# Optimization experiments

Measured on AMD Instinct MI355X. Metric: run time of the kernel, lower is better.

The kernel has to match this reference:

```python
import jax, jax.numpy as jnp
import numpy as np

B, N, F, T = 16, 1024, 32, 12
K, FC, FT, TS, D = 3, 64, 64, 1, 16
THETA_THR = 0.6
LN_EPS = 1e-5


def setup_inputs() -> dict:
    key = jax.random.key(0)
    ks = jax.random.split(key, 20)
    r = lambda i, shape, s=0.1: jax.random.normal(ks[i], shape, dtype=jnp.float32) * s
    return dict(
        x=jax.random.normal(ks[0], (B, N, F, T), dtype=jnp.float32),
        node_embeddings=r(1, (N, D), 1.0),
        W1=r(2, (T,)), W2=r(3, (F, T)), W3=r(4, (F,)),
        bs=r(5, (1, N, N)), Vs=r(6, (N, N)),
        U1=r(7, (N,)), U2=r(8, (F, N)), U3=r(9, (F,)),
        be=r(10, (1, T, T)), Ve=r(11, (T, T)),
        Theta=r(12, (K, F, FC)),
        tc_v=r(13, (FT, FC, 1, 3)), tc_g=jnp.ones((FT,), jnp.float32), tc_b=r(14, (FT,)),
        rc_w=r(15, (FT, F, 1, 1)), rc_b=r(16, (FT,)),
        ln_w=jnp.ones((FT,), jnp.float32), ln_b=jnp.zeros((FT,), jnp.float32),
    )


def _forward(x, node_embeddings, W1, W2, W3, bs, Vs, U1, U2, U3, be, Ve,
             Theta, tc_v, tc_g, tc_b, rc_w, rc_b, ln_w, ln_b):
    b, n, f, t = x.shape
    k_order = Theta.shape[0]

    # --- temporal attention: E (B,T,T) ---
    lhs = jnp.einsum('bnft,n->btf', x, U1) @ U2                # (B,T,N)
    rhs = jnp.einsum('f,bnft->bnt', U3, x)                     # (B,N,T)
    prod = jnp.einsum('btn,bnu->btu', lhs, rhs)                # (B,T,T)
    E = jnp.einsum('ts,bsu->btu', Ve, jax.nn.sigmoid(prod + be))
    E = jax.nn.softmax(E, axis=1)

    # x_TAt = reshape(B, N*F, T) @ E  (equivalent einsum over t)
    x_TAt = jnp.einsum('bnft,btu->bnfu', x, E)                 # (B,N,F,T)

    # --- sparse spatial attention on x_TAt: (B,N,N) ---
    l2 = jnp.einsum('bnft,t->bnf', x_TAt, W1) @ W2             # (B,N,T)
    r2 = jnp.einsum('f,bnft->btn', W3, x_TAt)                  # (B,T,N)
    prod2 = jnp.einsum('bnt,btm->bnm', l2, r2)                 # (B,N,N)
    S = jnp.einsum('nm,bmk->bnk', Vs, jax.nn.sigmoid(prod2 + bs))
    Sn = jax.nn.softmax(S, axis=1)
    thr = jnp.mean(Sn) / THETA_THR
    spat = jnp.where(Sn < thr, jnp.zeros_like(Sn), Sn)         # Sparse_S_normalized

    # --- K-order adaptive graph conv with attention mask ---
    sup = jax.nn.softmax(jax.nn.relu(node_embeddings @ node_embeddings.T), axis=1)
    polys = [jnp.eye(n, dtype=x.dtype), sup]
    for k in range(2, k_order):
        polys.append(2.0 * sup @ polys[-1] - polys[-2])
    out = jnp.zeros((b, t, n, Theta.shape[2]), x.dtype)
    for k in range(k_order):
        A = polys[k][None] * spat                              # (B,N,N)
        h = jnp.einsum('bnm,bnft->btmf', A, x)                 # A^T @ x per timestep
        out = out + jnp.einsum('btmf,fo->btmo', h, Theta[k])
    gcn = jax.nn.relu(out)                                     # (B,T,N,FC)

    # --- time conv (weight-normed 1x3) + residual 1x1 conv ---
    vnorm = jnp.sqrt(jnp.sum(tc_v * tc_v, axis=(1, 2, 3), keepdims=True))
    w = tc_g[:, None, None, None] * tc_v / vnorm
    inp = gcn.transpose(0, 3, 2, 1)                            # (B,FC,N,T)
    tco = jax.lax.conv_general_dilated(
        inp, w, (1, TS), ((0, 0), (1, 1)),
        dimension_numbers=('NCHW', 'OIHW', 'NCHW')) + tc_b[None, :, None, None]
    res = jax.lax.conv_general_dilated(
        x.transpose(0, 2, 1, 3), rc_w, (1, TS), ((0, 0), (0, 0)),
        dimension_numbers=('NCHW', 'OIHW', 'NCHW')) + rc_b[None, :, None, None]

    # --- layernorm over channel dim ---
    y = (res + tco).transpose(0, 3, 2, 1)                      # (B,T,N,FT)
    mu = jnp.mean(y, axis=-1, keepdims=True)
    var = jnp.var(y, axis=-1, keepdims=True)
    y = (y - mu) / jnp.sqrt(var + LN_EPS) * ln_w + ln_b
    x_res = y.transpose(0, 2, 3, 1)                            # (B,N,FT,T)
    return x_res, spat


def reference(x, node_embeddings, W1, W2, W3, bs, Vs, U1, U2, U3, be, Ve,
              Theta, tc_v, tc_g, tc_b, rc_w, rc_b, ln_w, ln_b):
    return _forward(x, node_embeddings, W1, W2, W3, bs, Vs, U1, U2, U3, be, Ve,
                    Theta, tc_v, tc_g, tc_b, rc_w, rc_b, ln_w, ln_b)
```

## Files before the change

### kernel.cpp

```cpp
#include <hip/hip_runtime.h>
#include <math.h>

#define NB 16
#define NN 1024
#define NF 32
#define NT 12
#define NFC 64
#define NFT 64

typedef __attribute__((ext_vector_type(8))) short bf16x8;
typedef __attribute__((ext_vector_type(4))) float f32x4;

__device__ inline unsigned short cvt_bf(float f) {
    unsigned int u = __float_as_uint(f);
    u += 0x7fff + ((u >> 16) & 1);
    return (unsigned short)(u >> 16);
}
__device__ inline float bf2f(unsigned short u) {
    return __uint_as_float(((unsigned int)u) << 16);
}
__device__ inline void gll16(const short* g, short* l) {
    __builtin_amdgcn_global_load_lds((const __attribute__((address_space(1))) void*)g,
                                     (__attribute__((address_space(3))) void*)l, 16, 0, 0);
}

__global__ __launch_bounds__(384) void k_pre(const float* __restrict__ x,
                                             const float* __restrict__ U1,
                                             const float* __restrict__ U3,
                                             const float* __restrict__ W3,
                                             float* __restrict__ lhs_pre,
                                             float* __restrict__ rhs,
                                             float* __restrict__ rr3,
                                             unsigned short* __restrict__ Xrow)
{
    __shared__ float xs[8 * 384];
    int b = blockIdx.x, ch = blockIdx.y, tid = threadIdx.x;
    float acc = 0.f;
    for (int c8 = 0; c8 < 8; c8++) {
        int n0 = ch * 64 + c8 * 8;
        size_t r0 = (size_t)b * NN + n0;
        __syncthreads();
        for (int i = 0; i < 8; i++) xs[i * 384 + tid] = x[(r0 + i) * 384 + tid];
        __syncthreads();
        for (int i = 0; i < 8; i++) acc += xs[i * 384 + tid] * U1[n0 + i];
        for (int idx = tid; idx < 1536; idx += 384) {
            int row = idx / 192, jj = (idx - row * 192) * 2;
            unsigned int w = (unsigned int)cvt_bf(xs[row * 384 + jj])
                           | ((unsigned int)cvt_bf(xs[row * 384 + jj + 1]) << 16);
            *(unsigned int*)(Xrow + (r0 + row) * 384 + jj) = w;
        }
        if (tid < 192) {
            int half = tid / 96;
            int r = tid - half * 96;
            int i = r / 12, t = r - i * 12;
            const float* wv = half ? W3 : U3;
            float s = 0.f;
            for (int f = 0; f < 32; f++) s += wv[f] * xs[i * 384 + f * 12 + t];
            float* outp = half ? rr3 : rhs;
            outp[(r0 + i) * 12 + t] = s;
        }
    }
    int f = tid / 12, t = tid - f * 12;
    atomicAdd(&lhs_pre[b * 384 + t * 32 + f], acc);
}

__global__ __launch_bounds__(384) void k_M2(const float* __restrict__ U2,
                                            const float* __restrict__ rhs,
                                            float* __restrict__ M2)
{
    int b = blockIdx.x, ch = blockIdx.y, tid = threadIdx.x;
    int f = tid / 12, u = tid - (tid / 12) * 12;
    int n0 = ch * 32;
    float a = 0.f;
    for (int n = n0; n < n0 + 32; n++)
        a += U2[(size_t)f * NN + n] * rhs[((size_t)b * NN + n) * 12 + u];
    atomicAdd(&M2[b * 384 + f * 12 + u], a);
}

__global__ __launch_bounds__(192) void k_E(const float* __restrict__ lhs_pre,
                                           const float* __restrict__ M2,
                                           const float* __restrict__ be,
                                           const float* __restrict__ Ve,
                                           const float* __restrict__ W1,
                                           float* __restrict__ E,
                                           float* __restrict__ EW1)
{
    int b = blockIdx.x, tid = threadIdx.x;
    __shared__ float lp2[384], m2s[384];
    __shared__ float ssig[144], sE[144], mx[12], sm[12];
    for (int i = tid; i < 384; i += 192) {
        lp2[i] = lhs_pre[b * 384 + i];
        m2s[i] = M2[b * 384 + i];
    }
    __syncthreads();
    if (tid < 144) {
        int s = tid / 12, u = tid - s * 12;
        float p = 0.f;
#pragma unroll
        for (int f = 0; f < 32; f++) p += lp2[s * 32 + f] * m2s[f * 12 + u];
        ssig[tid] = 1.f / (1.f + expf(-(p + be[tid])));
    }
    __syncthreads();
    if (tid < 144) {
        int t = tid / 12, u = tid - t * 12;
        float a = 0.f;
        for (int s2 = 0; s2 < 12; s2++) a += Ve[t * 12 + s2] * ssig[s2 * 12 + u];
        sE[tid] = a;
    }
    __syncthreads();
    if (tid < 12) {
        float m = -1e30f;
        for (int t = 0; t < 12; t++) m = fmaxf(m, sE[t * 12 + tid]);
        float s = 0.f;
        for (int t = 0; t < 12; t++) s += expf(sE[t * 12 + tid] - m);
        mx[tid] = m; sm[tid] = s;
    }
    __syncthreads();
    float val = 0.f;
    if (tid < 144) {
        int u = tid % 12;
        val = expf(sE[tid] - mx[u]) / sm[u];
        E[b * 144 + tid] = val;
    }
    __syncthreads();
    if (tid < 144) sE[tid] = val;
    __syncthreads();
    if (tid < 12) {
        float a = 0.f;
        for (int u = 0; u < 12; u++) a += sE[tid * 12 + u] * W1[u];
        EW1[b * 12 + tid] = a;
    }
}

__global__ __launch_bounds__(384) void k_l2r2x(const unsigned short* __restrict__ Xrow,
                                               const float* __restrict__ rr3,
                                               const float* __restrict__ E,
                                               const float* __restrict__ EW1,
                                               const float* __restrict__ W2,
                                               float* __restrict__ l2,
                                               float* __restrict__ r2)
{
    __shared__ float xs[8 * 384];
    __shared__ float Es[144], ew[12], rrs[96], lp[8][32];
    int b = blockIdx.y, tid = threadIdx.x;
    int n0 = blockIdx.x * 8;
    size_t r0 = (size_t)b * NN + n0;
    if (tid < 144) Es[tid] = E[b * 144 + tid];
    if (tid < 12) ew[tid] = EW1[b * 12 + tid];
    if (tid < 96) rrs[tid] = rr3[(r0 + tid / 12) * 12 + (tid % 12)];
    const unsigned int* Xr = (const unsigned int*)(Xrow + r0 * 384);
    for (int i2 = tid; i2 < 1536; i2 += 384) {
        unsigned int w = Xr[i2];
        xs[2 * i2]     = bf2f((unsigned short)(w & 0xffff));
        xs[2 * i2 + 1] = bf2f((unsigned short)(w >> 16));
    }
    __syncthreads();
    if (tid < 256) {
        int i = tid >> 5, f = tid & 31;
        float a = 0.f;
#pragma unroll
        for (int t = 0; t < 12; t++) a += xs[i * 384 + f * 12 + t] * ew[t];
        lp[i][f] = a;
    }
    __syncthreads();
    if (tid < 96) {
        int i = tid / 12, u = tid - i * 12;
        float a = 0.f;
        for (int f = 0; f < 32; f++) a += lp[i][f] * W2[f * 12 + u];
        l2[(r0 + i) * 12 + u] = a;
        float rv = 0.f;
#pragma unroll
        for (int t = 0; t < 12; t++) rv += rrs[i * 12 + t] * Es[t * 12 + u];
        r2[((size_t)b * 12 + u) * NN + n0 + i] = rv;
    }
}

__global__ __launch_bounds__(256) void k_xt(const unsigned short* __restrict__ Xrow,
                                            unsigned short* __restrict__ Xt,
                                            const float* __restrict__ Vs,
                                            unsigned short* __restrict__ Vsb)
{
    int tid = threadIdx.x;
    int fid = blockIdx.x + 6 * (blockIdx.y + 16 * blockIdx.z);
    if (fid < 1024) {
        size_t i = (size_t)fid * 1024 + tid * 4;
        float4 v = *(const float4*)(Vs + i);
        unsigned int p0 = (unsigned int)cvt_bf(v.x) | ((unsigned int)cvt_bf(v.y) << 16);
        unsigned int p1 = (unsigned int)cvt_bf(v.z) | ((unsigned int)cvt_bf(v.w) << 16);
        *(unsigned int*)(Vsb + i) = p0;
        *(unsigned int*)(Vsb + i + 2) = p1;
    }
    __shared__ unsigned short tl[64][66];
    int b = blockIdx.z;
    int n0 = blockIdx.y * 64, j0 = blockIdx.x * 64;
    int c = tid & 63, r0 = tid >> 6;
    for (int i = 0; i < 16; i++) {
        int r = r0 + i * 4;
        tl[r][c] = Xrow[((size_t)b * NN + n0 + r) * 384 + j0 + c];
    }
    __syncthreads();
    int c2 = tid & 31, r4 = tid >> 5;
    unsigned short* ob = Xt + ((size_t)b * 384 + j0) * NN + n0;
    for (int i = 0; i < 8; i++) {
        int jr = r4 + i * 8;
        unsigned int v0 = (unsigned int)tl[2 * c2][jr] | ((unsigned int)tl[2 * c2 + 1][jr] << 16);
        *(unsigned int*)(ob + (size_t)jr * NN + 2 * c2) = v0;
    }
}

__global__ __launch_bounds__(256) void k_Ptile(const float* __restrict__ l2,
                                               const float* __restrict__ r2,
                                               const float* __restrict__ bsin,
                                               unsigned short* __restrict__ Pt)
{
    __shared__ float l2s[64][13];
    __shared__ float r2s[12][64];
    __shared__ float bsS[64][65];
    int k0 = blockIdx.x * 64, m0 = blockIdx.y * 64, b = blockIdx.z;
    int tid = threadIdx.x;
    for (int i = tid; i < 768; i += 256) {
        int r = i / 12, t = i - r * 12;
        l2s[r][t] = l2[((size_t)b * NN + m0 + r) * 12 + t];
    }
    for (int i = tid; i < 768; i += 256) {
        int t = i >> 6, k = i & 63;
        r2s[t][k] = r2[((size_t)b * 12 + t) * NN + k0 + k];
    }
    for (int i = tid; i < 4096; i += 256) {
        int r = i >> 6, c = i & 63;
        bsS[r][c] = bsin[(size_t)(m0 + r) * NN + k0 + c];
    }
    __syncthreads();
    int m = tid & 63, kg = tid >> 6;
    float lv[12];
#pragma unroll
    for (int t = 0; t < 12; t++) lv[t] = l2s[m][t];
#pragma unroll
    for (int s = 0; s < 16; s++) {
        int kl = kg * 16 + s;
        float p = bsS[m][kl];
#pragma unroll
        for (int t = 0; t < 12; t++) p += lv[t] * r2s[t][kl];
        float sg = 1.f / (1.f + expf(-p));
        Pt[((size_t)b * NN + k0 + kl) * NN + m0 + m] = cvt_bf(sg);
    }
}

__global__ __launch_bounds__(256) void k_tb16(const unsigned short* __restrict__ s,
                                              unsigned short* __restrict__ d)
{
    __shared__ unsigned short tl[64][65];
    int r0 = blockIdx.y * 64, c0 = blockIdx.x * 64;
    int tid = threadIdx.x;
    int c = tid & 63, rr = tid >> 6;
    for (int i = 0; i < 16; i++)
        tl[rr + i * 4][c] = s[(size_t)(r0 + rr + i * 4) * NN + c0 + c];
    __syncthreads();
    for (int i = 0; i < 16; i++)
        d[(size_t)(c0 + rr + i * 4) * NN + r0 + c] = tl[c][rr + i * 4];
}

__device__ inline void stage2(const short* __restrict__ g, int grow0, int gk0,
                              short* dstbase, int tid)
{
#pragma unroll
    for (int o = 0; o < 2; o++) {
        int y = o * 8192 + tid * 16;
        int rowh = y >> 7;
        int colb = (y & 127) ^ ((rowh & 7) << 4);
        const short* src = g + (size_t)(grow0 + rowh) * NN + gk0 + (colb >> 1);
        gll16(src, dstbase + (y >> 1));
    }
}

__global__ __launch_bounds__(512, 2) void sgemm8(const short* __restrict__ A,
                                                 const short* __restrict__ Bm,
                                                 float* __restrict__ C,
                                                 float* __restrict__ colsum)
{
    int bz = blockIdx.z;
    const short* Bb = Bm + (size_t)bz * NN * NN;
    int i0 = blockIdx.y * 256, j0 = blockIdx.x * 256;
    __shared__ short sm[65536];
    int tid = threadIdx.x;
    int ln = tid & 63, wv = tid >> 6;
    int wm = (wv >> 2) * 128, wn = (wv & 3) * 64;
    int fr = ln & 15, fk = ln >> 4;
    int ahalf = wv >> 2;
    int bhalf = wn >> 7;
    int bcol = wn & 64;
    int swz = (fr & 7) << 4;
    int kcol0 = ((fk * 16) ^ swz) >> 1;
    int kcol1 = ((64 + fk * 16) ^ swz) >> 1;

    f32x4 acc[8][4];
#pragma unroll
    for (int m = 0; m < 8; m++)
#pragma unroll
        for (int n = 0; n < 4; n++) acc[m][n] = (f32x4)(0.f);

    stage2(Bb, j0 + 0,   0,  sm + 16384,        tid);
    stage2(Bb, j0 + 128, 0,  sm + 16384 + 8192, tid);
    stage2(A,  i0 + 0,   0,  sm + 0,            tid);
    stage2(A,  i0 + 128, 0,  sm + 8192,         tid);
    stage2(Bb, j0 + 0,   64, sm + 32768 + 16384,        tid);
    stage2(Bb, j0 + 128, 64, sm + 32768 + 16384 + 8192, tid);
    asm volatile("s_waitcnt vmcnt(4)" ::: "memory");
    __builtin_amdgcn_s_barrier();

    for (int i = 0; i < 8; i++) {
        bf16x8 bv[8];
#pragma unroll
        for (int ph = 0; ph < 8; ph++) {
            int t = 2 * i + (ph >> 2);
            int p = t & 1;
            int q = ph & 3;
            int abase = p * 32768 + ahalf * 8192;
            int bbase = p * 32768 + 16384 + bhalf * 8192;
            if (q == 0) {
#pragma unroll
                for (int nj = 0; nj < 4; nj++) {
                    int browh = bcol + nj * 16 + fr;
                    bv[nj * 2 + 0] = *(const bf16x8*)(sm + bbase + browh * 64 + kcol0);
                    bv[nj * 2 + 1] = *(const bf16x8*)(sm + bbase + browh * 64 + kcol1);
                }
            }
            bf16x8 av[4];
#pragma unroll
            for (int m2 = 0; m2 < 2; m2++) {
                int rowh = (2 * q + m2) * 16 + fr;
                av[m2 * 2 + 0] = *(const bf16x8*)(sm + abase + rowh * 64 + kcol0);
                av[m2 * 2 + 1] = *(const bf16x8*)(sm + abase + rowh * 64 + kcol1);
            }
            {
                int st, smat, shalf;
                if (ph == 0)      { st = 2 * i + 1; smat = 0; shalf = 0; }
                else if (ph == 1) { st = 2 * i + 1; smat = 0; shalf = 1; }
                else if (ph == 2) { st = 2 * i + 2; smat = 1; shalf = 0; }
                else if (ph == 3) { st = 2 * i + 2; smat = 1; shalf = 1; }
                else if (ph == 4) { st = 2 * i + 2; smat = 0; shalf = 0; }
                else if (ph == 5) { st = 2 * i + 2; smat = 0; shalf = 1; }
                else if (ph == 6) { st = 2 * i + 3; smat = 1; shalf = 0; }
                else              { st = 2 * i + 3; smat = 1; shalf = 1; }
                if (st < 16) {
                    short* dst = sm + (st & 1) * 32768 + smat * 16384 + shalf * 8192;
                    const short* g = smat ? Bb : A;
                    int grow0 = (smat ? j0 : i0) + shalf * 128;
                    stage2(g, grow0, st * 64, dst, tid);
                }
            }
            __builtin_amdgcn_s_barrier();
            __builtin_amdgcn_s_setprio(1);
#pragma unroll
            for (int m2 = 0; m2 < 2; m2++)
#pragma unroll
                for (int nj = 0; nj < 4; nj++) {
                    acc[2 * q + m2][nj] = __builtin_amdgcn_mfma_f32_16x16x32_bf16(
                        av[m2 * 2 + 0], bv[nj * 2 + 0], acc[2 * q + m2][nj], 0, 0, 0);
                    acc[2 * q + m2][nj] = __builtin_amdgcn_mfma_f32_16x16x32_bf16(
                        av[m2 * 2 + 1], bv[nj * 2 + 1], acc[2 * q + m2][nj], 0, 0, 0);
                }
            __builtin_amdgcn_s_setprio(0);
            if (ph == 3 || ph == 7) {
                if (i < 7) asm volatile("s_waitcnt vmcnt(4)" ::: "memory");
                else       asm volatile("s_waitcnt vmcnt(0)" ::: "memory");
            }
            __builtin_amdgcn_s_barrier();
        }
    }
    float* Cb = C + (size_t)bz * NN * NN;
#pragma unroll
    for (int nj = 0; nj < 4; nj++) {
        int col = j0 + wn + nj * 16 + fr;
        float cs = 0.f;
#pragma unroll
        for (int m = 0; m < 8; m++) {
            int row = i0 + wm + m * 16 + fk * 4;
#pragma unroll
            for (int r = 0; r < 4; r++) {
                float e = expf(acc[m][nj][r]);
                Cb[(size_t)(row + r) * NN + col] = e;
                cs += e;
            }
        }
        cs += __shfl_xor(cs, 16);
        cs += __shfl_xor(cs, 32);
        if (ln < 16) atomicAdd(&colsum[(size_t)bz * NN + col], cs);
    }
}

template<int MODE>
__global__ __launch_bounds__(256) void mgemm(const short* __restrict__ A,
                                             const short* __restrict__ B,
                                             void* __restrict__ Cv,
                                             int Kd, int kchunk,
                                             int ldA, int ldB, int ldC,
                                             long sA, long sB, long sC,
                                             float* __restrict__ colsum)
{
    int bz = blockIdx.z;
    const short* Ab = A + (size_t)bz * sA;
    const short* Bb = B + (size_t)bz * sB;
    int i0 = blockIdx.y * 128, j0 = blockIdx.x * 128;
    __shared__ short sm[16384];
    int tid = threadIdx.x;
    int ln = tid & 63, wv = tid >> 6;
    int wm = (wv >> 1) * 64, wn = (wv & 1) * 64;
    int fr = ln & 15, fk = ln >> 4;
    f32x4 acc[4][4];
#pragma unroll
    for (int a = 0; a < 4; a++)
#pragma unroll
        for (int b2 = 0; b2 < 4; b2++) acc[a][b2] = (f32x4)(0.f);

    int k_lo = 0, k_hi = Kd;
    if constexpr (MODE == 3) { k_lo = bz * kchunk; k_hi = k_lo + kchunk; }

    for (int k0 = k_lo; k0 < k_hi; k0 += 64) {
#pragma unroll
        for (int q = 0; q < 4; q++) {
            int e = q * 2048 + tid * 8;
            const short* src = Ab + (size_t)(i0 + (e >> 6)) * ldA + k0 + (e & 63);
            gll16(src, sm + e);
        }
#pragma unroll
        for (int q = 0; q < 4; q++) {
            int e = q * 2048 + tid * 8;
            const short* src = Bb + (size_t)(j0 + (e >> 6)) * ldB + k0 + (e & 63);
            gll16(src, sm + 8192 + e);
        }
        __syncthreads();
#pragma unroll
        for (int ks = 0; ks < 2; ks++) {
            bf16x8 av[4], bv[4];
#pragma unroll
            for (int mi = 0; mi < 4; mi++)
                av[mi] = *(const bf16x8*)(sm + (wm + mi * 16 + fr) * 64 + ks * 32 + fk * 8);
#pragma unroll
            for (int nj = 0; nj < 4; nj++)
                bv[nj] = *(const bf16x8*)(sm + 8192 + (wn + nj * 16 + fr) * 64 + ks * 32 + fk * 8);
#pragma unroll
            for (int mi = 0; mi < 4; mi++)
#pragma unroll
                for (int nj = 0; nj < 4; nj++)
                    acc[mi][nj] = __builtin_amdgcn_mfma_f32_16x16x32_bf16(av[mi], bv[nj], acc[mi][nj], 0, 0, 0);
        }
        __syncthreads();
    }
    if constexpr (MODE == 3) {
        float* Cb = (float*)Cv;
#pragma unroll
        for (int mi = 0; mi < 4; mi++)
#pragma unroll
            for (int nj = 0; nj < 4; nj++) {
                int row = i0 + wm + mi * 16 + fk * 4;
                int col = j0 + wn + nj * 16 + fr;
#pragma unroll
                for (int r = 0; r < 4; r++)
                    atomicAdd(&Cb[(size_t)(row + r) * ldC + col], acc[mi][nj][r]);
            }
    }
}

__global__ __launch_bounds__(256) void mgemm_hh(const short* __restrict__ A1,
                                                const short* __restrict__ A2,
                                                const short* __restrict__ B,
                                                unsigned short* __restrict__ C1,
                                                unsigned short* __restrict__ C2)
{
    int id = blockIdx.x;
    int half = id / 384;
    int sid = id - half * 384;
    int xcd = sid & 7, jj = sid >> 3;
    int b = (xcd << 1) | (jj / 24);
    int r = jj % 24;
    int i0 = (r / 3) * 128, j0 = (r % 3) * 128;
    const short* Ab = (half ? A2 : A1) + (size_t)b * NN * NN;
    const short* Bb = B + (size_t)b * 384 * NN;
    unsigned short* C = half ? C2 : C1;
    __shared__ short sm[16384];
    int tid = threadIdx.x;
    int ln = tid & 63, wv = tid >> 6;
    int wm = (wv >> 1) * 64, wn = (wv & 1) * 64;
    int fr = ln & 15, fk = ln >> 4;
    f32x4 acc[4][4];
#pragma unroll
    for (int a = 0; a < 4; a++)
#pragma unroll
        for (int b2 = 0; b2 < 4; b2++) acc[a][b2] = (f32x4)(0.f);

    for (int k0 = 0; k0 < NN; k0 += 64) {
#pragma unroll
        for (int q = 0; q < 4; q++) {
            int e = q * 2048 + tid * 8;
            gll16(Ab + (size_t)(i0 + (e >> 6)) * NN + k0 + (e & 63), sm + e);
        }
#pragma unroll
        for (int q = 0; q < 4; q++) {
            int e = q * 2048 + tid * 8;
            gll16(Bb + (size_t)(j0 + (e >> 6)) * NN + k0 + (e & 63), sm + 8192 + e);
        }
        __syncthreads();
#pragma unroll
        for (int ks = 0; ks < 2; ks++) {
            bf16x8 av[4], bv[4];
#pragma unroll
            for (int mi = 0; mi < 4; mi++)
                av[mi] = *(const bf16x8*)(sm + (wm + mi * 16 + fr) * 64 + ks * 32 + fk * 8);
#pragma unroll
            for (int nj = 0; nj < 4; nj++)
                bv[nj] = *(const bf16x8*)(sm + 8192 + (wn + nj * 16 + fr) * 64 + ks * 32 + fk * 8);
#pragma unroll
            for (int mi = 0; mi < 4; mi++)
#pragma unroll
                for (int nj = 0; nj < 4; nj++)
                    acc[mi][nj] = __builtin_amdgcn_mfma_f32_16x16x32_bf16(av[mi], bv[nj], acc[mi][nj], 0, 0, 0);
        }
        __syncthreads();
    }
#pragma unroll
    for (int mi = 0; mi < 4; mi++)
#pragma unroll
        for (int nj = 0; nj < 4; nj++) {
            int row = i0 + wm + mi * 16 + fk * 4;
            int col = j0 + wn + nj * 16 + fr;
#pragma unroll
            for (int r2 = 0; r2 < 4; r2++)
                C[((size_t)b * NN + row + r2) * 384 + col] = cvt_bf(acc[mi][nj][r2]);
        }
}

__global__ __launch_bounds__(256) void k_normprep2(float* __restrict__ spat,
                                                   const float* __restrict__ colsum,
                                                   const float* __restrict__ sup,
                                                   const float* __restrict__ supsq,
                                                   unsigned short* __restrict__ At1,
                                                   unsigned short* __restrict__ At2,
                                                   float* __restrict__ sdiag)
{
    __shared__ unsigned short t1[64][66];
    __shared__ unsigned short t2[64][66];
    int b = blockIdx.z;
    int n0 = blockIdx.y * 64, m0 = blockIdx.x * 64;
    int tid = threadIdx.x;
    int c = tid & 63, r0 = tid >> 6;
    const float thr = (1.0f / 1024.0f) / 0.6f;
    float inv = 1.f / colsum[(size_t)b * NN + m0 + c];
    float* sp = spat + (size_t)b * NN * NN;
    for (int i = 0; i < 16; i++) {
        int r = r0 + i * 4;
        size_t idx = (size_t)(n0 + r) * NN + m0 + c;
        float v = sp[idx] * inv;
        v = (v < thr) ? 0.f : v;
        sp[idx] = v;
        if (n0 + r == m0 + c) sdiag[(size_t)b * NN + n0 + r] = v;
        t1[r][c] = cvt_bf(sup[(size_t)(n0 + r) * NN + m0 + c] * v);
        float p2 = 2.f * supsq[(size_t)(n0 + r) * NN + m0 + c]
                 - (((n0 + r) == (m0 + c)) ? 1.f : 0.f);
        t2[r][c] = cvt_bf(p2 * v);
    }
    __syncthreads();
    int c2 = tid & 31, r4 = tid >> 5;
    size_t ob = ((size_t)b * NN + m0) * NN + n0;
    for (int i = 0; i < 8; i++) {
        int rr = r4 + i * 8;
        unsigned int v1 = (unsigned int)t1[2 * c2][rr] | ((unsigned int)t1[2 * c2 + 1][rr] << 16);
        unsigned int v2 = (unsigned int)t2[2 * c2][rr] | ((unsigned int)t2[2 * c2 + 1][rr] << 16);
        *(unsigned int*)(At1 + ob + (size_t)rr * NN + 2 * c2) = v1;
        *(unsigned int*)(At2 + ob + (size_t)rr * NN + 2 * c2) = v2;
    }
}

__global__ __launch_bounds__(256) void k_sup(const float* __restrict__ emb,
                                             float* __restrict__ sup,
                                             unsigned short* __restrict__ supB)
{
    int n = blockIdx.x, tid = threadIdx.x;
    __shared__ float en[16];
    if (tid < 16) en[tid] = emb[n * 16 + tid];
    __syncthreads();
    float v[4];
#pragma unroll
    for (int q = 0; q < 4; q++) {
        int m = q * 256 + tid;
        float d = 0.f;
#pragma unroll
        for (int dd = 0; dd < 16; dd++) d += en[dd] * emb[m * 16 + dd];
        v[q] = fmaxf(d, 0.f);
    }
    float mx = fmaxf(fmaxf(v[0], v[1]), fmaxf(v[2], v[3]));
    for (int o = 32; o > 0; o >>= 1) mx = fmaxf(mx, __shfl_xor(mx, o));
    __shared__ float red[4];
    if ((tid & 63) == 0) red[tid >> 6] = mx;
    __syncthreads();
    mx = fmaxf(fmaxf(red[0], red[1]), fmaxf(red[2], red[3]));
    float e[4];
    float s = 0.f;
#pragma unroll
    for (int q = 0; q < 4; q++) { e[q] = expf(v[q] - mx); s += e[q]; }
    for (int o = 32; o > 0; o >>= 1) s += __shfl_xor(s, o);
    __shared__ float red2[4];
    if ((tid & 63) == 0) red2[tid >> 6] = s;
    __syncthreads();
    s = red2[0] + red2[1] + red2[2] + red2[3];
    float inv = 1.f / s;
#pragma unroll
    for (int q = 0; q < 4; q++) {
        float val = e[q] * inv;
        sup[(size_t)n * NN + q * 256 + tid] = val;
        supB[(size_t)n * NN + q * 256 + tid] = cvt_bf(val);
    }
}

__global__ __launch_bounds__(256) void k_wprep(const float* __restrict__ tcv,
                                               const float* __restrict__ tcg,
                                               const float* __restrict__ Theta,
                                               const float* __restrict__ rcw,
                                               unsigned short* __restrict__ Wr,
                                               unsigned short* __restrict__ Th,
                                               unsigned short* __restrict__ Rc)
{
    int tid = threadIdx.x;
    if (blockIdx.x < 64) {
        int o = blockIdx.x;
        float t = 0.f, p = 0.f;
        if (tid < 192) { t = tcv[o * 192 + tid]; p = t * t; }
        for (int off = 32; off > 0; off >>= 1) p += __shfl_xor(p, off);
        __shared__ float wsr[3];
        if (tid < 192 && (tid & 63) == 0) wsr[tid >> 6] = p;
        __syncthreads();
        if (tid < 192) {
            float sum = wsr[0] + wsr[1] + wsr[2];
            int c = tid / 3, dt = tid - c * 3;
            Wr[o * 192 + dt * 64 + c] = cvt_bf(t * (tcg[o] / sqrtf(sum)));
        }
    } else {
        for (int i = tid; i < 6144; i += 256) {
            int o = i / 96, rem = i - o * 96;
            int kind = rem >> 5, f = rem & 31;
            Th[i] = cvt_bf(Theta[kind * 2048 + f * 64 + o]);
        }
        for (int i = tid; i < 2048; i += 256) Rc[i] = cvt_bf(rcw[i]);
    }
}

__global__ __launch_bounds__(256) void k_tail(const float* __restrict__ x,
                                              const unsigned short* __restrict__ h1,
                                              const unsigned short* __restrict__ h2,
                                              const float* __restrict__ sdiag,
                                              const unsigned short* __restrict__ Th,
                                              const unsigned short* __restrict__ Wr,
                                              const unsigned short* __restrict__ Rc,
                                              const float* __restrict__ tcb,
                                              const float* __restrict__ rcb,
                                              const float* __restrict__ lnw,
                                              const float* __restrict__ lnb,
                                              float* __restrict__ out)
{
    int b = blockIdx.y;
    int node0 = blockIdx.x * 4;
    int tid = threadIdx.x;
    int ln = tid & 63, wv = tid >> 6;
    int fr = ln & 15, fk = ln >> 4;

    __shared__ union {
        struct { unsigned short xt[1920], h1t[1920], h2t[1920], gcn[4032]; } a;
        float Y[48 * 65];
    } u;
    __shared__ float sdp[48];
    __shared__ float lnwS[64], lnbS[64], tbS[64];
    __shared__ float muS[48], rsS[48];

    size_t rowb = ((size_t)b * NN + node0) * 384;
    {
        const float2* xp = (const float2*)(x + rowb);
        const unsigned int* h1p = (const unsigned int*)(h1 + rowb);
        const unsigned int* h2p = (const unsigned int*)(h2 + rowb);
        for (int q = tid; q < 768; q += 256) {
            int j0 = q * 2;
            int node = j0 / 384, j = j0 - node * 384;
            int f = j / 12, t = j - f * 12;
            int t2 = t + 1, f2 = f;
            if (t2 == 12) { t2 = 0; f2 = f + 1; }
            int la0 = node * 480 + t * 40 + f;
            int la1 = node * 480 + t2 * 40 + f2;
            float2 xv = xp[q];
            unsigned int w1 = h1p[q], w2 = h2p[q];
            u.a.xt[la0] = cvt_bf(xv.x);  u.a.xt[la1] = cvt_bf(xv.y);
            u.a.h1t[la0] = (unsigned short)(w1 & 0xffff); u.a.h1t[la1] = (unsigned short)(w1 >> 16);
            u.a.h2t[la0] = (unsigned short)(w2 & 0xffff); u.a.h2t[la1] = (unsigned short)(w2 >> 16);
        }
    }
    for (int i = tid; i < 576; i += 256) {
        int node = i / 144, r = i - node * 144;
        int rr = (r < 72) ? 0 : 13;
        u.a.gcn[node * 1008 + rr * 72 + (r % 72)] = 0;
    }
    if (tid < 48) sdp[tid] = sdiag[(size_t)b * NN + node0 + tid / 12];
    if (tid < 64) { lnwS[tid] = lnw[tid]; lnbS[tid] = lnb[tid]; tbS[tid] = tcb[tid] + rcb[tid]; }

    int ocol = wv * 16 + fr;
    bf16x8 bTh[3], bWr[6], bRc;
#pragma unroll
    for (int kb = 0; kb < 3; kb++)
        bTh[kb] = *(const bf16x8*)((const short*)Th + (size_t)ocol * 96 + kb * 32 + fk * 8);
#pragma unroll
    for (int kb = 0; kb < 6; kb++)
        bWr[kb] = *(const bf16x8*)((const short*)Wr + (size_t)ocol * 192 + kb * 32 + fk * 8);
    bRc = *(const bf16x8*)((const short*)Rc + (size_t)ocol * 32 + fk * 8);

    int na[3], ta[3];
#pragma unroll
    for (int rb = 0; rb < 3; rb++) {
        int p = rb * 16 + fr;
        na[rb] = p / 12; ta[rb] = p - na[rb] * 12;
    }
    __syncthreads();

    f32x4 acc[3];
#pragma unroll
    for (int rb = 0; rb < 3; rb++) {
        int ax = na[rb] * 480 + ta[rb] * 40 + fk * 8;
        bf16x8 avx = *(const bf16x8*)(u.a.xt + ax);
        f32x4 z = (f32x4)(0.f);
        acc[rb] = __builtin_amdgcn_mfma_f32_16x16x32_bf16(avx, bTh[0], z, 0, 0, 0);
#pragma unroll
        for (int r = 0; r < 4; r++) acc[rb][r] *= sdp[rb * 16 + fk * 4 + r];
        bf16x8 av1 = *(const bf16x8*)(u.a.h1t + ax);
        acc[rb] = __builtin_amdgcn_mfma_f32_16x16x32_bf16(av1, bTh[1], acc[rb], 0, 0, 0);
        bf16x8 av2 = *(const bf16x8*)(u.a.h2t + ax);
        acc[rb] = __builtin_amdgcn_mfma_f32_16x16x32_bf16(av2, bTh[2], acc[rb], 0, 0, 0);
    }
#pragma unroll
    for (int rb = 0; rb < 3; rb++) {
#pragma unroll
        for (int r = 0; r < 4; r++) {
            int pc = rb * 16 + fk * 4 + r;
            int nc = pc / 12, tc2 = pc - nc * 12;
            u.a.gcn[nc * 1008 + (tc2 + 1) * 72 + wv * 16 + fr] = cvt_bf(fmaxf(acc[rb][r], 0.f));
        }
    }
    __syncthreads();
#pragma unroll
    for (int rb = 0; rb < 3; rb++) {
        f32x4 a2 = (f32x4)(0.f);
#pragma unroll
        for (int kb = 0; kb < 6; kb++) {
            int dt = kb >> 1, c0 = (kb & 1) * 32;
            bf16x8 ag = *(const bf16x8*)(u.a.gcn + na[rb] * 1008 + (ta[rb] + dt) * 72 + c0 + fk * 8);
            a2 = __builtin_amdgcn_mfma_f32_16x16x32_bf16(ag, bWr[kb], a2, 0, 0, 0);
        }
        int ax = na[rb] * 480 + ta[rb] * 40 + fk * 8;
        bf16x8 avx = *(const bf16x8*)(u.a.xt + ax);
        acc[rb] = __builtin_amdgcn_mfma_f32_16x16x32_bf16(avx, bRc, a2, 0, 0, 0);
    }
    __syncthreads();
    float tb = tbS[ocol];
#pragma unroll
    for (int rb = 0; rb < 3; rb++)
#pragma unroll
        for (int r = 0; r < 4; r++)
            u.Y[(rb * 16 + fk * 4 + r) * 65 + ocol] = acc[rb][r] + tb;
    __syncthreads();
    if (tid < 48) {
        float s = 0.f, s2 = 0.f;
        for (int o = 0; o < 64; o++) {
            float v = u.Y[tid * 65 + o];
            s += v; s2 += v * v;
        }
        float mm = s * (1.f / 64.f);
        float var = s2 * (1.f / 64.f) - mm * mm;
        muS[tid] = mm; rsS[tid] = rsqrtf(var + 1e-5f);
    }
    __syncthreads();
    float2* obv = (float2*)(out + rowb * 2);
    for (int q = tid; q < 1536; q += 256) {
        int i = q * 2;
        int node = i / 768, rr = i - node * 768;
        int o = rr / 12, t = rr - o * 12;
        int p0 = node * 12 + t;
        float v0 = (u.Y[p0 * 65 + o] - muS[p0]) * rsS[p0] * lnwS[o] + lnbS[o];
        int t1 = t + 1, o1 = o;
        if (t1 == 12) { t1 = 0; o1 = o + 1; }
        int p1 = node * 12 + t1;
        float v1 = (u.Y[p1 * 65 + o1] - muS[p1]) * rsS[p1] * lnwS[o1] + lnbS[o1];
        float2 pk; pk.x = v0; pk.y = v1;
        obv[q] = pk;
    }
}

extern "C" void kernel_launch(void* const* d_in, const int* in_sizes, int n_in,
                              void* d_out, int out_size, void* d_ws, size_t ws_size,
                              hipStream_t stream)
{
    const float* x    = (const float*)d_in[0];
    const float* emb  = (const float*)d_in[1];
    const float* W1   = (const float*)d_in[2];
    const float* W2   = (const float*)d_in[3];
    const float* W3   = (const float*)d_in[4];
    const float* bs   = (const float*)d_in[5];
    const float* Vs   = (const float*)d_in[6];
    const float* U1   = (const float*)d_in[7];
    const float* U2   = (const float*)d_in[8];
    const float* U3   = (const float*)d_in[9];
    const float* be   = (const float*)d_in[10];
    const float* Ve   = (const float*)d_in[11];
    const float* Theta= (const float*)d_in[12];
    const float* tcv  = (const float*)d_in[13];
    const float* tcg  = (const float*)d_in[14];
    const float* tcb  = (const float*)d_in[15];
    const float* rcw  = (const float*)d_in[16];
    const float* rcb  = (const float*)d_in[17];
    const float* lnw  = (const float*)d_in[18];
    const float* lnb  = (const float*)d_in[19];

    float* xres = (float*)d_out;
    float* spat = xres + (size_t)NB * NN * NFT * NT;

    char* base = (char*)d_ws;
    unsigned short* Xrow = (unsigned short*)(base + 0);
    unsigned short* Pt   = (unsigned short*)(base + 0);
    unsigned short* supB = (unsigned short*)(base + 0);
    unsigned short* supT = (unsigned short*)(base + 2097152);
    unsigned short* At1  = (unsigned short*)(base + 0);
    unsigned short* At2  = (unsigned short*)xres;
    unsigned short* Xt  = (unsigned short*)(base + 33554432);
    unsigned short* h1  = (unsigned short*)(base + 46137344);
    unsigned short* h2  = (unsigned short*)(base + 58720256);
    unsigned short* Vsb = (unsigned short*)(base + 71303168);
    float* colsum  = (float*)(base + 73400320);
    float* sdiag   = (float*)(base + 73465856);
    float* sup     = (float*)(base + 77594624);
    float* supsq   = (float*)(base + 81788928);
    float* lhs_pre = (float*)(base + 85983232);
    float* M2      = (float*)(base + 86007808);
    float* rhs     = (float*)(base + 86794240);
    float* rr3     = (float*)(base + 87580672);
    float* E       = (float*)(base + 88376320);
    float* EW1     = (float*)(base + 88385536);
    float* l2      = (float*)(base + 88386560);
    float* r2      = (float*)(base + 89172992);
    unsigned short* Wr = (unsigned short*)(base + 89959424);
    unsigned short* Th = (unsigned short*)(base + 89984000);
    unsigned short* Rc = (unsigned short*)(base + 89996288);

    hipMemsetAsync(lhs_pre, 0, 49152, stream);
    hipMemsetAsync(supsq, 0, (size_t)NN * NN * sizeof(float), stream);

    k_pre<<<dim3(16, 16), 384, 0, stream>>>(x, U1, U3, W3, lhs_pre, rhs, rr3, Xrow);
    k_M2<<<dim3(16, 32), 384, 0, stream>>>(U2, rhs, M2);
    k_E<<<16, 192, 0, stream>>>(lhs_pre, M2, be, Ve, W1, E, EW1);
    k_l2r2x<<<dim3(128, 16), 384, 0, stream>>>(Xrow, rr3, E, EW1, W2, l2, r2);
    k_xt<<<dim3(6, 16, 16), 256, 0, stream>>>(Xrow, Xt, Vs, Vsb);
    k_Ptile<<<dim3(16, 16, 16), 256, 0, stream>>>(l2, r2, bs, Pt);
    hipMemsetAsync(colsum, 0, (size_t)NB * NN * sizeof(float), stream);
    sgemm8<<<dim3(4, 4, 16), 512, 0, stream>>>((const short*)Vsb, (const short*)Pt,
                                               spat, colsum);
    k_sup<<<1024, 256, 0, stream>>>(emb, sup, supB);
    k_tb16<<<dim3(16, 16), 256, 0, stream>>>(supB, supT);
    mgemm<3><<<dim3(8, 8, 4), 256, 0, stream>>>((const short*)supB, (const short*)supT,
        (void*)supsq, NN, 256, NN, NN, NN, 0L, 0L, 0L, nullptr);
    k_normprep2<<<dim3(16, 16, 16), 256, 0, stream>>>(spat, colsum, sup, supsq, At1, At2, sdiag);
    mgemm_hh<<<768, 256, 0, stream>>>((const short*)At1, (const short*)At2,
                                      (const short*)Xt, h1, h2);
    k_wprep<<<65, 256, 0, stream>>>(tcv, tcg, Theta, rcw, Wr, Th, Rc);
    k_tail<<<dim3(256, 16), 256, 0, stream>>>(x, h1, h2, sdiag, Th, Wr, Rc,
                                              tcb, rcb, lnw, lnb, xres);
}
```

Measured before the change: 290.4 us.

## Store exp scores as bf16 scratch, reuse bf16 x rows in tail

The spatial GEMM epilogue now writes exp(S) as bf16 into a separate scratch buffer instead of fp32 into the output, which halves that write. The normalization kernel reads that bf16 buffer, and its block indexing is reordered so batch is the fastest grid dimension. The tail kernel reads the already converted bf16 Xrow instead of the fp32 x, and the workspace is re-laid out so these buffers no longer alias. The normalized attention is now computed from bf16-rounded exponentials, which can change which values fall under the sparsity threshold.

New measurement: 304.1 us. 1.05x slower.

```diff
diff --git a/kernel.cpp b/kernel.cpp
--- a/kernel.cpp
+++ b/kernel.cpp
@@ -275,7 +275,7 @@
 
 __global__ __launch_bounds__(512, 2) void sgemm8(const short* __restrict__ A,
                                                  const short* __restrict__ Bm,
-                                                 float* __restrict__ C,
+                                                 unsigned short* __restrict__ expB,
                                                  float* __restrict__ colsum)
 {
     int bz = blockIdx.z;
@@ -368,7 +368,7 @@
             __builtin_amdgcn_s_barrier();
         }
     }
-    float* Cb = C + (size_t)bz * NN * NN;
+    unsigned short* Cb = expB + (size_t)bz * NN * NN;
 #pragma unroll
     for (int nj = 0; nj < 4; nj++) {
         int col = j0 + wn + nj * 16 + fr;
@@ -379,7 +379,7 @@
 #pragma unroll
             for (int r = 0; r < 4; r++) {
                 float e = expf(acc[m][nj][r]);
-                Cb[(size_t)(row + r) * NN + col] = e;
+                Cb[(size_t)(row + r) * NN + col] = cvt_bf(e);
                 cs += e;
             }
         }
@@ -530,7 +530,8 @@
         }
 }
 
-__global__ __launch_bounds__(256) void k_normprep2(float* __restrict__ spat,
+__global__ __launch_bounds__(256) void k_normprep2(const unsigned short* __restrict__ expB,
+                                                   float* __restrict__ spat,
                                                    const float* __restrict__ colsum,
                                                    const float* __restrict__ sup,
                                                    const float* __restrict__ supsq,
@@ -540,17 +541,18 @@
 {
     __shared__ unsigned short t1[64][66];
     __shared__ unsigned short t2[64][66];
-    int b = blockIdx.z;
-    int n0 = blockIdx.y * 64, m0 = blockIdx.x * 64;
+    int b = blockIdx.x;
+    int m0 = blockIdx.y * 64, n0 = blockIdx.z * 64;
     int tid = threadIdx.x;
     int c = tid & 63, r0 = tid >> 6;
     const float thr = (1.0f / 1024.0f) / 0.6f;
     float inv = 1.f / colsum[(size_t)b * NN + m0 + c];
+    const unsigned short* eb = expB + (size_t)b * NN * NN;
     float* sp = spat + (size_t)b * NN * NN;
     for (int i = 0; i < 16; i++) {
         int r = r0 + i * 4;
         size_t idx = (size_t)(n0 + r) * NN + m0 + c;
-        float v = sp[idx] * inv;
+        float v = bf2f(eb[idx]) * inv;
         v = (v < thr) ? 0.f : v;
         sp[idx] = v;
         if (n0 + r == m0 + c) sdiag[(size_t)b * NN + n0 + r] = v;
@@ -644,7 +646,7 @@
     }
 }
 
-__global__ __launch_bounds__(256) void k_tail(const float* __restrict__ x,
+__global__ __launch_bounds__(256) void k_tail(const unsigned short* __restrict__ Xrow,
                                               const unsigned short* __restrict__ h1,
                                               const unsigned short* __restrict__ h2,
                                               const float* __restrict__ sdiag,
@@ -673,7 +675,7 @@
 
     size_t rowb = ((size_t)b * NN + node0) * 384;
     {
-        const float2* xp = (const float2*)(x + rowb);
+        const unsigned int* xp = (const unsigned int*)(Xrow + rowb);
         const unsigned int* h1p = (const unsigned int*)(h1 + rowb);
         const unsigned int* h2p = (const unsigned int*)(h2 + rowb);
         for (int q = tid; q < 768; q += 256) {
@@ -684,9 +686,8 @@
             if (t2 == 12) { t2 = 0; f2 = f + 1; }
             int la0 = node * 480 + t * 40 + f;
             int la1 = node * 480 + t2 * 40 + f2;
-            float2 xv = xp[q];
-            unsigned int w1 = h1p[q], w2 = h2p[q];
-            u.a.xt[la0] = cvt_bf(xv.x);  u.a.xt[la1] = cvt_bf(xv.y);
+            unsigned int wx = xp[q], w1 = h1p[q], w2 = h2p[q];
+            u.a.xt[la0] = (unsigned short)(wx & 0xffff); u.a.xt[la1] = (unsigned short)(wx >> 16);
             u.a.h1t[la0] = (unsigned short)(w1 & 0xffff); u.a.h1t[la1] = (unsigned short)(w1 >> 16);
             u.a.h2t[la0] = (unsigned short)(w2 & 0xffff); u.a.h2t[la1] = (unsigned short)(w2 >> 16);
         }
@@ -819,30 +820,31 @@
 
     char* base = (char*)d_ws;
     unsigned short* Xrow = (unsigned short*)(base + 0);
-    unsigned short* Pt   = (unsigned short*)(base + 0);
-    unsigned short* supB = (unsigned short*)(base + 0);
-    unsigned short* supT = (unsigned short*)(base + 2097152);
-    unsigned short* At1  = (unsigned short*)(base + 0);
+    unsigned short* Pt   = (unsigned short*)(base + 16777216);
+    unsigned short* expB = (unsigned short*)(base + 56623104);
+    unsigned short* At1  = (unsigned short*)(base + 96468992);
     unsigned short* At2  = (unsigned short*)xres;
-    unsigned short* Xt  = (unsigned short*)(base + 33554432);
-    unsigned short* h1  = (unsigned short*)(base + 46137344);
-    unsigned short* h2  = (unsigned short*)(base + 58720256);
-    unsigned short* Vsb = (unsigned short*)(base + 71303168);
-    float* colsum  = (float*)(base + 73400320);
-    float* sdiag   = (float*)(base + 73465856);
-    float* sup     = (float*)(base + 77594624);
-    float* supsq   = (float*)(base + 81788928);
-    float* lhs_pre = (float*)(base + 85983232);
-    float* M2      = (float*)(base + 86007808);
-    float* rhs     = (float*)(base + 86794240);
-    float* rr3     = (float*)(base + 87580672);
-    float* E       = (float*)(base + 88376320);
-    float* EW1     = (float*)(base + 88385536);
-    float* l2      = (float*)(base + 88386560);
-    float* r2      = (float*)(base + 89172992);
-    unsigned short* Wr = (unsigned short*)(base + 89959424);
-    unsigned short* Th = (unsigned short*)(base + 89984000);
-    unsigned short* Rc = (unsigned short*)(base + 89996288);
+    unsigned short* Xt   = (unsigned short*)(base + 134217728);
+    unsigned short* h1   = (unsigned short*)(base + 150994944);
+    unsigned short* h2   = (unsigned short*)(base + 167772160);
+    unsigned short* Vsb  = (unsigned short*)(base + 184549376);
+    float* colsum  = (float*)(base + 188743680);
+    float* sdiag   = (float*)(base + 188809216);
+    float* sup     = (float*)(base + 192937984);
+    unsigned short* supB = (unsigned short*)(base + 197132288);
+    unsigned short* supT = (unsigned short*)(base + 199229440);
+    float* supsq   = (float*)(base + 201326592);
+    float* lhs_pre = (float*)(base + 205520896);
+    float* M2      = (float*)(base + 205545472);
+    float* rhs     = (float*)(base + 205570048);
+    float* rr3     = (float*)(base + 206356480);
+    float* E       = (float*)(base + 207142912);
+    float* EW1     = (float*)(base + 207152128);
+    float* l2      = (float*)(base + 207153152);
+    float* r2      = (float*)(base + 207939584);
+    unsigned short* Wr = (unsigned short*)(base + 208726016);
+    unsigned short* Th = (unsigned short*)(base + 208750592);
+    unsigned short* Rc = (unsigned short*)(base + 208762880);
 
     hipMemsetAsync(lhs_pre, 0, 49152, stream);
     hipMemsetAsync(supsq, 0, (size_t)NN * NN * sizeof(float), stream);
@@ -855,15 +857,16 @@
     k_Ptile<<<dim3(16, 16, 16), 256, 0, stream>>>(l2, r2, bs, Pt);
     hipMemsetAsync(colsum, 0, (size_t)NB * NN * sizeof(float), stream);
     sgemm8<<<dim3(4, 4, 16), 512, 0, stream>>>((const short*)Vsb, (const short*)Pt,
-                                               spat, colsum);
+                                               expB, colsum);
     k_sup<<<1024, 256, 0, stream>>>(emb, sup, supB);
     k_tb16<<<dim3(16, 16), 256, 0, stream>>>(supB, supT);
     mgemm<3><<<dim3(8, 8, 4), 256, 0, stream>>>((const short*)supB, (const short*)supT,
         (void*)supsq, NN, 256, NN, NN, NN, 0L, 0L, 0L, nullptr);
-    k_normprep2<<<dim3(16, 16, 16), 256, 0, stream>>>(spat, colsum, sup, supsq, At1, At2, sdiag);
+    k_normprep2<<<dim3(16, 16, 16), 256, 0, stream>>>(expB, spat, colsum, sup, supsq,
+                                                      At1, At2, sdiag);
     mgemm_hh<<<768, 256, 0, stream>>>((const short*)At1, (const short*)At2,
                                       (const short*)Xt, h1, h2);
     k_wprep<<<65, 256, 0, stream>>>(tcv, tcg, Theta, rcw, Wr, Th, Rc);
-    k_tail<<<dim3(256, 16), 256, 0, stream>>>(x, h1, h2, sdiag, Th, Wr, Rc,
+    k_tail<<<dim3(256, 16), 256, 0, stream>>>(Xrow, h1, h2, sdiag, Th, Wr, Rc,
                                               tcb, rcb, lnw, lnb, xres);
 }
```
